# Kernel optimization log

Measured on AMD Instinct MI355X. Metric: run time of the kernel, lower is better.

The kernel has to match this reference:

```python
import jax, jax.numpy as jnp
import numpy as np

NUM_HEADS = 32
KV_HEADS = 8
HEAD_SIZE = 128
BATCH = 32
BLOCK_SIZE = 16
BLOCKS_PER_SEQ = 128
NUM_BLOCKS = BATCH * BLOCKS_PER_SEQ  # 4096
ROPE_BASE = 10000.0


def _rope(x, pos):
    # x: [B, n_heads, D]; pos: [B] int32 -> rotate per-sequence single token
    d = x.shape[-1]
    inv_freq = 1.0 / (ROPE_BASE ** (jnp.arange(0, d, 2, dtype=jnp.float32) / d))  # [D/2]
    freqs = pos.astype(jnp.float32)[:, None] * inv_freq[None, :]                  # [B, D/2]
    emb = jnp.concatenate([freqs, freqs], axis=-1)                                # [B, D]
    cos = jnp.cos(emb)[:, None, :]
    sin = jnp.sin(emb)[:, None, :]
    x1, x2 = x[..., : d // 2], x[..., d // 2 :]
    rotated = jnp.concatenate([-x2, x1], axis=-1)
    return x * cos + rotated * sin


def setup_inputs() -> dict:
    key = jax.random.key(0)
    ks = jax.random.split(key, 6)
    query = jax.random.normal(ks[0], (BATCH, NUM_HEADS, HEAD_SIZE), dtype=jnp.float32)
    k_new = jax.random.normal(ks[1], (BATCH, KV_HEADS, HEAD_SIZE), dtype=jnp.float32)
    v_new = jax.random.normal(ks[2], (BATCH, KV_HEADS, HEAD_SIZE), dtype=jnp.float32)
    k_cache = jax.random.normal(ks[3], (NUM_BLOCKS, BLOCK_SIZE, KV_HEADS, HEAD_SIZE), dtype=jnp.float32)
    v_cache = jax.random.normal(ks[4], (NUM_BLOCKS, BLOCK_SIZE, KV_HEADS, HEAD_SIZE), dtype=jnp.float32)
    # each sequence owns a contiguous run of blocks
    block_tables = jnp.arange(NUM_BLOCKS, dtype=jnp.int32).reshape(BATCH, BLOCKS_PER_SEQ)
    context_lens = jax.random.randint(ks[5], (BATCH,), 0, 2047, dtype=jnp.int32)
    return {
        "query": query,
        "key": k_new,
        "value": v_new,
        "k_cache": k_cache,
        "v_cache": v_cache,
        "block_tables": block_tables,
        "context_lens": context_lens,
    }


def reference(query, key, value, k_cache, v_cache, block_tables, context_lens):
    B, H, D = query.shape
    KVH = key.shape[1]
    G = H // KVH
    scale = 1.0 / (D ** 0.5)

    # --- RoPE: source uses position = context_len + 1 for both q and k ---
    pos = context_lens + 1
    q = _rope(query, pos)   # [B, H, D]
    k = _rope(key, pos)     # [B, KVH, D]

    # --- scatter new token into the paged KV cache at slot = context_len ---
    slot = context_lens                               # [B]
    blk = jnp.take_along_axis(block_tables, (slot // BLOCK_SIZE)[:, None], axis=1)[:, 0]
    off = slot % BLOCK_SIZE
    k_cache = k_cache.at[blk, off].set(k)
    v_cache = v_cache.at[blk, off].set(value)

    # --- gather this batch's pages: [B, T, KVH, D] with T = blocks*block_size ---
    T = BLOCKS_PER_SEQ * BLOCK_SIZE
    K = k_cache[block_tables].reshape(B, T, KVH, D)
    V = v_cache[block_tables].reshape(B, T, KVH, D)

    # --- GQA single-query attention over cache_seqlens = context_len + 1 ---
    qg = q.reshape(B, KVH, G, D)
    scores = jnp.einsum("bhgd,bthd->bhgt", qg, K) * scale            # [B, KVH, G, T]
    valid = (jnp.arange(T, dtype=jnp.int32)[None, :] < (context_lens + 1)[:, None])
    scores = jnp.where(valid[:, None, None, :], scores, -jnp.inf)
    probs = jax.nn.softmax(scores, axis=-1)
    out = jnp.einsum("bhgt,bthd->bhgd", probs, V)                    # [B, KVH, G, D]
    return out.reshape(B, H, D)
```

## Files before the change

kernel.cpp:

```cpp
#include <hip/hip_runtime.h>
#include <math.h>

#define BATCH    32
#define NHEADS   32
#define KVHEADS  8
#define GRP      4
#define HSZ      128
#define BLKSZ    16
#define BPS      128
#define NTHREADS 512
#define NPROC    16
#define CHUNK    256
#define NSPLIT   8
#define SCALE    0.08838834764831843f

__device__ __forceinline__ void dot4(float4& acc, const float* qb, const float4 k) {
    const float4 qa = *(const float4*)(qb);
    const float4 qg = *(const float4*)(qb + HSZ);
    const float4 qc = *(const float4*)(qb + 2 * HSZ);
    const float4 qd = *(const float4*)(qb + 3 * HSZ);
    acc.x = fmaf(qa.x,k.x,fmaf(qa.y,k.y,fmaf(qa.z,k.z,fmaf(qa.w,k.w,acc.x))));
    acc.y = fmaf(qg.x,k.x,fmaf(qg.y,k.y,fmaf(qg.z,k.z,fmaf(qg.w,k.w,acc.y))));
    acc.z = fmaf(qc.x,k.x,fmaf(qc.y,k.y,fmaf(qc.z,k.z,fmaf(qc.w,k.w,acc.z))));
    acc.w = fmaf(qd.x,k.x,fmaf(qd.y,k.y,fmaf(qd.z,k.z,fmaf(qd.w,k.w,acc.w))));
}

__device__ __forceinline__ void red2(float4& a) {
    a.x += __shfl_xor(a.x,1); a.x += __shfl_xor(a.x,2);
    a.y += __shfl_xor(a.y,1); a.y += __shfl_xor(a.y,2);
    a.z += __shfl_xor(a.z,1); a.z += __shfl_xor(a.z,2);
    a.w += __shfl_xor(a.w,1); a.w += __shfl_xor(a.w,2);
}

__device__ __forceinline__ void pvfma(float4* o, const float4 pv, const float4 vv) {
    o[0].x += pv.x*vv.x; o[0].y += pv.x*vv.y; o[0].z += pv.x*vv.z; o[0].w += pv.x*vv.w;
    o[1].x += pv.y*vv.x; o[1].y += pv.y*vv.y; o[1].z += pv.y*vv.z; o[1].w += pv.y*vv.w;
    o[2].x += pv.z*vv.x; o[2].y += pv.z*vv.y; o[2].z += pv.z*vv.z; o[2].w += pv.z*vv.w;
    o[3].x += pv.w*vv.x; o[3].y += pv.w*vv.y; o[3].z += pv.w*vv.z; o[3].w += pv.w*vv.w;
}

__global__ __launch_bounds__(NTHREADS, 8) void pa_partial(
    const float* __restrict__ query,
    const float* __restrict__ k_new,
    const float* __restrict__ v_new,
    const float* __restrict__ k_cache,
    const float* __restrict__ v_cache,
    const int*  __restrict__ block_tables,
    const int*  __restrict__ ctx_lens,
    float* __restrict__ pm, float* __restrict__ pl, float* __restrict__ po)
{
    const int wg    = blockIdx.x;
    const int chunk = wg & (NSPLIT - 1);
    const int kvh   = (wg >> 3) & (KVHEADS - 1);
    const int b     = wg >> 6;
    const int ctx   = ctx_lens[b];
    const int t0    = chunk * CHUNK;
    if (t0 > ctx) return;

    const int tid  = threadIdx.x;
    const int lane = tid & 63;
    const int wave = tid >> 6;

    __shared__ float q_s[GRP][HSZ];
    __shared__ float kn_s[HSZ];
    __shared__ int   bt_s[CHUNK / BLKSZ];
    __shared__ float sp[CHUNK][GRP];
    __shared__ float redm[8], redl[8];
    __shared__ float o_s[NPROC][GRP][HSZ];

    {
        float* s1 = &sp[0][0];
        s1[tid]       = -INFINITY;
        s1[tid + 512] = -INFINITY;
    }
    {
        const float p = (float)(ctx + 1);
        if (tid < 320) {
            const int   i    = tid & 63;
            const float invf = exp2f(-((float)i / 64.0f) * 13.287712379549449f);
            float s_, c_;
            sincosf(p * invf, &s_, &c_);
            if (tid < 256) {
                const int g = tid >> 6;
                const float* qp = query + ((size_t)b * NHEADS + kvh * GRP + g) * HSZ;
                const float x1 = qp[i], x2 = qp[i + 64];
                q_s[g][i]      = (x1 * c_ - x2 * s_) * SCALE;
                q_s[g][i + 64] = (x2 * c_ + x1 * s_) * SCALE;
            } else {
                const float* kp = k_new + ((size_t)b * KVHEADS + kvh) * HSZ;
                const float x1 = kp[i], x2 = kp[i + 64];
                kn_s[i]      = x1 * c_ - x2 * s_;
                kn_s[i + 64] = x2 * c_ + x1 * s_;
            }
        } else if (tid < 320 + CHUNK / BLKSZ) {
            bt_s[tid - 320] = block_tables[b * BPS + (t0 >> 4) + (tid - 320)];
        }
    }
    __syncthreads();

    const int ncache = min(t0 + CHUNK, ctx) - t0;

    const int rg = lane >> 2;
    const int j  = lane & 3;
    const int jo = j << 2;

    {
        const int tA0 = wave * 16;
        const int tB0 = 128 + wave * 16;
        if (tB0 < ncache) {
            const float* kra = k_cache + (((size_t)bt_s[tA0 >> 4] * BLKSZ + rg) * KVHEADS + kvh) * HSZ + jo;
            const float* krb = k_cache + (((size_t)bt_s[tB0 >> 4] * BLKSZ + rg) * KVHEADS + kvh) * HSZ + jo;
            float4 ka[8], kb[8];
#pragma unroll
            for (int u = 0; u < 8; ++u) ka[u] = *(const float4*)(kra + u * 16);
#pragma unroll
            for (int u = 0; u < 8; ++u) kb[u] = *(const float4*)(krb + u * 16);
            float4 aA = make_float4(0.f,0.f,0.f,0.f);
            float4 aB = make_float4(0.f,0.f,0.f,0.f);
#pragma unroll
            for (int u = 0; u < 8; ++u) {
                const float* qb = &q_s[0][u * 16 + jo];
                dot4(aA, qb, ka[u]);
                dot4(aB, qb, kb[u]);
            }
            red2(aA); red2(aB);
            if (j == 0) {
                *(float4*)&sp[tA0 + rg][0] = aA;
                if (tB0 + rg < ncache) *(float4*)&sp[tB0 + rg][0] = aB;
            }
        } else if (tA0 < ncache) {
            const float* kra = k_cache + (((size_t)bt_s[tA0 >> 4] * BLKSZ + rg) * KVHEADS + kvh) * HSZ + jo;
            float4 ka[8];
#pragma unroll
            for (int u = 0; u < 8; ++u) ka[u] = *(const float4*)(kra + u * 16);
            float4 aA = make_float4(0.f,0.f,0.f,0.f);
#pragma unroll
            for (int u = 0; u < 8; ++u) dot4(aA, &q_s[0][u * 16 + jo], ka[u]);
            red2(aA);
            if (j == 0 && tA0 + rg < ncache) *(float4*)&sp[tA0 + rg][0] = aA;
        }
    }
    if (chunk == (ctx >> 8) && wave == 0) {
        const int tc = ctx - t0;
        float4 acc = make_float4(0.f,0.f,0.f,0.f);
#pragma unroll
        for (int u = 0; u < 8; ++u) {
            const float4 kv = *(const float4*)&kn_s[u * 16 + jo];
            dot4(acc, &q_s[0][u * 16 + jo], kv);
        }
        red2(acc);
        if (lane == 0) *(float4*)&sp[tc][0] = acc;
    }
    __syncthreads();

    const int g2 = tid >> 7;
    const int t2 = (tid & 127) << 1;
    const float a0 = sp[t2][g2], a1 = sp[t2 + 1][g2];
    float mx = fmaxf(a0, a1);
    mx = fmaxf(mx, __shfl_xor(mx, 1));
    mx = fmaxf(mx, __shfl_xor(mx, 2));
    mx = fmaxf(mx, __shfl_xor(mx, 4));
    mx = fmaxf(mx, __shfl_xor(mx, 8));
    mx = fmaxf(mx, __shfl_xor(mx, 16));
    mx = fmaxf(mx, __shfl_xor(mx, 32));
    if ((tid & 63) == 0) redm[tid >> 6] = mx;
    __syncthreads();
    const float m_g = fmaxf(redm[g2 << 1], redm[(g2 << 1) + 1]);
    const float p0 = __expf(a0 - m_g);
    const float p1 = __expf(a1 - m_g);
    sp[t2][g2]     = p0;
    sp[t2 + 1][g2] = p1;
    float ls = p0 + p1;
    ls += __shfl_xor(ls, 1);
    ls += __shfl_xor(ls, 2);
    ls += __shfl_xor(ls, 4);
    ls += __shfl_xor(ls, 8);
    ls += __shfl_xor(ls, 16);
    ls += __shfl_xor(ls, 32);
    if ((tid & 63) == 0) redl[tid >> 6] = ls;
    __syncthreads();
    const float l_g = redl[g2 << 1] + redl[(g2 << 1) + 1];

    const int sub  = tid & 31;
    const int proc = tid >> 5;
    const int d0   = sub << 2;
    float4 o[GRP];
#pragma unroll
    for (int g = 0; g < GRP; ++g) o[g] = make_float4(0.f,0.f,0.f,0.f);
    {
        float4 v0 = make_float4(0.f,0.f,0.f,0.f);
        float4 v1 = v0;
        #define VADDR(tt, fb) (v_cache + (((size_t)bt_s[(((tt) < ncache) ? (tt) : (fb)) >> 4] * BLKSZ \
                              + ((((tt) < ncache) ? (tt) : (fb)) & 15)) * KVHEADS + kvh) * HSZ + d0)
        if (proc < ncache) {
            v0 = *(const float4*)VADDR(proc, proc);
            v1 = *(const float4*)VADDR(proc + 16, proc);
            for (int t = proc; t < ncache; t += NPROC) {
                const float4 vn = *(const float4*)VADDR(t + 32, t);
                const float4 pv = *(const float4*)&sp[t][0];
                pvfma(o, pv, v0);
                v0 = v1; v1 = vn;
            }
        }
        #undef VADDR
    }
    if (chunk == (ctx >> 8)) {
        const int tc = ctx - t0;
        if (proc == (tc & (NPROC - 1))) {
            const float4 vn = *(const float4*)(v_new + ((size_t)b * KVHEADS + kvh) * HSZ + d0);
            const float4 pv = *(const float4*)&sp[tc][0];
            pvfma(o, pv, vn);
        }
    }

#pragma unroll
    for (int g = 0; g < GRP; ++g) *(float4*)&o_s[proc][g][d0] = o[g];
    __syncthreads();
    {
        const int g = tid >> 7;
        const int d = tid & 127;
        float acc = 0.f;
#pragma unroll
        for (int p = 0; p < NPROC; ++p) acc += o_s[p][g][d];
        const size_t idx = (((size_t)(b * KVHEADS + kvh)) * GRP + g) * NSPLIT + chunk;
        if (d == 0) { pm[idx] = m_g; pl[idx] = l_g; }
        po[idx * HSZ + d] = acc;
    }
}

__global__ __launch_bounds__(NTHREADS) void pa_reduce(
    const int*  __restrict__ ctx_lens,
    const float* __restrict__ pm, const float* __restrict__ pl,
    const float* __restrict__ po, float* __restrict__ out)
{
    const int b    = blockIdx.x >> 3;
    const int kvh  = blockIdx.x & 7;
    const int ctx  = ctx_lens[b];
    const int nact = (ctx >> 8) + 1;
    const int tid  = threadIdx.x;
    const int g    = tid >> 7;
    const int d    = tid & 127;
    const size_t idx = (((size_t)(b * KVHEADS + kvh)) * GRP + g) * NSPLIT;

    float M = -INFINITY;
    for (int p = 0; p < nact; ++p) M = fmaxf(M, pm[idx + p]);
    float L = 0.f, O = 0.f;
    for (int p = 0; p < nact; ++p) {
        const float w = __expf(pm[idx + p] - M);
        L += pl[idx + p] * w;
        O += po[(idx + p) * HSZ + d] * w;
    }
    out[((size_t)b * NHEADS + kvh * GRP + g) * HSZ + d] = O / L;
}

__device__ __forceinline__ float hsum32(float v) {
    v += __shfl_xor(v, 1); v += __shfl_xor(v, 2); v += __shfl_xor(v, 4);
    v += __shfl_xor(v, 8); v += __shfl_xor(v, 16);
    return v;
}
__device__ __forceinline__ void proc_row_f(const float4 kv, const float4 vv,
                                           const float4* qf, float* m, float* l, float4* o) {
    float s[GRP];
#pragma unroll
    for (int g = 0; g < GRP; ++g)
        s[g] = qf[g].x*kv.x + qf[g].y*kv.y + qf[g].z*kv.z + qf[g].w*kv.w;
#pragma unroll
    for (int g = 0; g < GRP; ++g) s[g] = hsum32(s[g]);
#pragma unroll
    for (int g = 0; g < GRP; ++g) {
        const float sc = s[g] * SCALE;
        const float mn = fmaxf(m[g], sc);
        const float cf = __expf(m[g] - mn);
        const float pp = __expf(sc - mn);
        l[g] = l[g] * cf + pp;
        o[g].x = o[g].x*cf + pp*vv.x; o[g].y = o[g].y*cf + pp*vv.y;
        o[g].z = o[g].z*cf + pp*vv.z; o[g].w = o[g].w*cf + pp*vv.w;
        m[g] = mn;
    }
}
__global__ __launch_bounds__(NTHREADS) void paged_attn_single(
    const float* __restrict__ query, const float* __restrict__ k_new,
    const float* __restrict__ v_new, const float* __restrict__ k_cache,
    const float* __restrict__ v_cache, const int* __restrict__ block_tables,
    const int* __restrict__ ctx_lens, float* __restrict__ out)
{
    const int wg = blockIdx.x, b = wg >> 3, kvh = wg & 7;
    const int tid = threadIdx.x, sub = tid & 31, proc = tid >> 5;
    const int ctx = ctx_lens[b];
    __shared__ float q_s[GRP][HSZ];
    __shared__ float kn_s[HSZ];
    __shared__ int   bt_s[BPS];
    __shared__ float m_s[16][GRP];
    __shared__ float l_s[16][GRP];
    __shared__ float o_s[16][GRP][HSZ];
    {
        const float p = (float)(ctx + 1);
        if (tid < 320) {
            const int   i    = tid & 63;
            const float invf = exp2f(-((float)i / 64.0f) * 13.287712379549449f);
            float s_, c_;
            sincosf(p * invf, &s_, &c_);
            if (tid < 256) {
                const int g = tid >> 6;
                const float* qp = query + ((size_t)b * NHEADS + kvh * GRP + g) * HSZ;
                const float x1 = qp[i], x2 = qp[i + 64];
                q_s[g][i] = x1*c_ - x2*s_; q_s[g][i+64] = x2*c_ + x1*s_;
            } else {
                const float* kp = k_new + ((size_t)b * KVHEADS + kvh) * HSZ;
                const float x1 = kp[i], x2 = kp[i + 64];
                kn_s[i] = x1*c_ - x2*s_; kn_s[i+64] = x2*c_ + x1*s_;
            }
        } else if (tid < 448) {
            bt_s[tid - 320] = block_tables[b * BPS + (tid - 320)];
        }
    }
    __syncthreads();
    const int d0 = sub << 2;
    float4 qf[GRP];
#pragma unroll
    for (int g = 0; g < GRP; ++g) qf[g] = *(const float4*)&q_s[g][d0];
    float m[GRP], l[GRP]; float4 o[GRP];
#pragma unroll
    for (int g = 0; g < GRP; ++g) { m[g] = -INFINITY; l[g] = 0.f; o[g] = make_float4(0,0,0,0); }
    for (int t = proc; t < ctx; t += 16) {
        const int blk = bt_s[t >> 4];
        const size_t a0 = (((size_t)blk*BLKSZ + (t & 15))*KVHEADS + kvh)*HSZ + d0;
        proc_row_f(*(const float4*)(k_cache + a0), *(const float4*)(v_cache + a0), qf, m, l, o);
    }
    if (proc == (ctx & 15)) {
        proc_row_f(*(const float4*)&kn_s[d0],
                   *(const float4*)(v_new + ((size_t)b*KVHEADS + kvh)*HSZ + d0), qf, m, l, o);
    }
    if (sub == 0) {
#pragma unroll
        for (int g = 0; g < GRP; ++g) { m_s[proc][g] = m[g]; l_s[proc][g] = l[g]; }
    }
#pragma unroll
    for (int g = 0; g < GRP; ++g) *(float4*)&o_s[proc][g][d0] = o[g];
    __syncthreads();
    {
        const int g = tid >> 7, d = tid & 127;
        float mt = -INFINITY;
#pragma unroll
        for (int p = 0; p < 16; ++p) mt = fmaxf(mt, m_s[p][g]);
        float lt = 0.f, ot = 0.f;
#pragma unroll
        for (int p = 0; p < 16; ++p) {
            const float wgt = __expf(m_s[p][g] - mt);
            lt += l_s[p][g]*wgt; ot += o_s[p][g][d]*wgt;
        }
        out[((size_t)b*NHEADS + kvh*GRP + g)*HSZ + d] = ot / lt;
    }
}

extern "C" void kernel_launch(void* const* d_in, const int* in_sizes, int n_in,
                              void* d_out, int out_size, void* d_ws, size_t ws_size,
                              hipStream_t stream) {
    const float* query        = (const float*)d_in[0];
    const float* k_new        = (const float*)d_in[1];
    const float* v_new        = (const float*)d_in[2];
    const float* k_cache      = (const float*)d_in[3];
    const float* v_cache      = (const float*)d_in[4];
    const int*   block_tables = (const int*)d_in[5];
    const int*   ctx_lens     = (const int*)d_in[6];
    float*       out          = (float*)d_out;

    const size_t NPART = (size_t)BATCH * KVHEADS * GRP * NSPLIT;
    const size_t need  = (NPART * 2 + NPART * HSZ) * sizeof(float);

    if (ws_size >= need) {
        float* pm = (float*)d_ws;
        float* pl = pm + NPART;
        float* po = pl + NPART;
        pa_partial<<<dim3(BATCH * KVHEADS * NSPLIT), dim3(NTHREADS), 0, stream>>>(
            query, k_new, v_new, k_cache, v_cache, block_tables, ctx_lens, pm, pl, po);
        pa_reduce<<<dim3(BATCH * KVHEADS), dim3(NTHREADS), 0, stream>>>(
            ctx_lens, pm, pl, po, out);
    } else {
        paged_attn_single<<<dim3(BATCH * KVHEADS), dim3(NTHREADS), 0, stream>>>(
            query, k_new, v_new, k_cache, v_cache, block_tables, ctx_lens, out);
    }
}
```

Measured before the change: 72.56 us.

## Split context into 64-token chunks and stage V in shared memory

Splits each sequence into 32 chunks of 64 tokens instead of 8 chunks of 256, and uses 256-thread workgroups, giving many more workgroups for latency hiding across the GPU. Each thread loads its K and V rows together in one pass, and V is staged in shared memory for the PV product. This replaces the separate strided V-prefetch loop and cross-wave o_s reduction. Softmax is now done per wave with a single 64-lane reduction. The cost is four times more partials for the reduce kernel and a larger workspace, which may trigger the single-kernel fallback if the workspace is too small.

```diff
diff --git a/kernel.cpp b/kernel.cpp
--- a/kernel.cpp
+++ b/kernel.cpp
@@ -8,11 +8,12 @@
 #define HSZ      128
 #define BLKSZ    16
 #define BPS      128
-#define NTHREADS 512
-#define NPROC    16
-#define CHUNK    256
-#define NSPLIT   8
+#define NTHREADS 256
+#define CHUNK    64
+#define NSPLIT   32
 #define SCALE    0.08838834764831843f
+
+#define NPART    ((size_t)BATCH * KVHEADS * GRP * NSPLIT)
 
 __device__ __forceinline__ void dot4(float4& acc, const float* qb, const float4 k) {
     const float4 qa = *(const float4*)(qb);
@@ -32,14 +33,7 @@
     a.w += __shfl_xor(a.w,1); a.w += __shfl_xor(a.w,2);
 }
 
-__device__ __forceinline__ void pvfma(float4* o, const float4 pv, const float4 vv) {
-    o[0].x += pv.x*vv.x; o[0].y += pv.x*vv.y; o[0].z += pv.x*vv.z; o[0].w += pv.x*vv.w;
-    o[1].x += pv.y*vv.x; o[1].y += pv.y*vv.y; o[1].z += pv.y*vv.z; o[1].w += pv.y*vv.w;
-    o[2].x += pv.z*vv.x; o[2].y += pv.z*vv.y; o[2].z += pv.z*vv.z; o[2].w += pv.z*vv.w;
-    o[3].x += pv.w*vv.x; o[3].y += pv.w*vv.y; o[3].z += pv.w*vv.z; o[3].w += pv.w*vv.w;
-}
-
-__global__ __launch_bounds__(NTHREADS, 8) void pa_partial(
+__global__ __launch_bounds__(NTHREADS, 4) void pa_partial(
     const float* __restrict__ query,
     const float* __restrict__ k_new,
     const float* __restrict__ v_new,
@@ -49,186 +43,128 @@
     const int*  __restrict__ ctx_lens,
     float* __restrict__ pm, float* __restrict__ pl, float* __restrict__ po)
 {
-    const int wg    = blockIdx.x;
-    const int chunk = wg & (NSPLIT - 1);
-    const int kvh   = (wg >> 3) & (KVHEADS - 1);
-    const int b     = wg >> 6;
+    const int chunk = blockIdx.x & (NSPLIT - 1);
+    const int kvh   = (blockIdx.x >> 5) & (KVHEADS - 1);
+    const int b     = blockIdx.x >> 8;
     const int ctx   = ctx_lens[b];
     const int t0    = chunk * CHUNK;
     if (t0 > ctx) return;
 
     const int tid  = threadIdx.x;
     const int lane = tid & 63;
-    const int wave = tid >> 6;
+    const int w    = tid >> 6;
 
     __shared__ float q_s[GRP][HSZ];
     __shared__ float kn_s[HSZ];
+    __shared__ float vt[CHUNK][HSZ + 4];
+    __shared__ float sp[CHUNK][GRP];
     __shared__ int   bt_s[CHUNK / BLKSZ];
-    __shared__ float sp[CHUNK][GRP];
-    __shared__ float redm[8], redl[8];
-    __shared__ float o_s[NPROC][GRP][HSZ];
-
-    {
-        float* s1 = &sp[0][0];
-        s1[tid]       = -INFINITY;
-        s1[tid + 512] = -INFINITY;
-    }
-    {
-        const float p = (float)(ctx + 1);
-        if (tid < 320) {
-            const int   i    = tid & 63;
-            const float invf = exp2f(-((float)i / 64.0f) * 13.287712379549449f);
-            float s_, c_;
-            sincosf(p * invf, &s_, &c_);
-            if (tid < 256) {
-                const int g = tid >> 6;
-                const float* qp = query + ((size_t)b * NHEADS + kvh * GRP + g) * HSZ;
-                const float x1 = qp[i], x2 = qp[i + 64];
-                q_s[g][i]      = (x1 * c_ - x2 * s_) * SCALE;
-                q_s[g][i + 64] = (x2 * c_ + x1 * s_) * SCALE;
-            } else {
-                const float* kp = k_new + ((size_t)b * KVHEADS + kvh) * HSZ;
-                const float x1 = kp[i], x2 = kp[i + 64];
-                kn_s[i]      = x1 * c_ - x2 * s_;
-                kn_s[i + 64] = x2 * c_ + x1 * s_;
-            }
-        } else if (tid < 320 + CHUNK / BLKSZ) {
-            bt_s[tid - 320] = block_tables[b * BPS + (t0 >> 4) + (tid - 320)];
-        }
-    }
-    __syncthreads();
-
-    const int ncache = min(t0 + CHUNK, ctx) - t0;
+
+    {
+        const int   i    = tid & 63;
+        const float p    = (float)(ctx + 1);
+        const float invf = exp2f(-((float)i / 64.0f) * 13.287712379549449f);
+        float s_, c_;
+        sincosf(p * invf, &s_, &c_);
+        const int g = tid >> 6;
+        const float* qp = query + ((size_t)b * NHEADS + kvh * GRP + g) * HSZ;
+        const float x1 = qp[i], x2 = qp[i + 64];
+        q_s[g][i]      = (x1 * c_ - x2 * s_) * SCALE;
+        q_s[g][i + 64] = (x2 * c_ + x1 * s_) * SCALE;
+        if (tid < 64) {
+            const float* kp = k_new + ((size_t)b * KVHEADS + kvh) * HSZ;
+            const float y1 = kp[i], y2 = kp[i + 64];
+            kn_s[i]      = y1 * c_ - y2 * s_;
+            kn_s[i + 64] = y2 * c_ + y1 * s_;
+        }
+        if (tid < CHUNK / BLKSZ) bt_s[tid] = block_tables[b * BPS + chunk * (CHUNK / BLKSZ) + tid];
+    }
+    __syncthreads();
+
+    const int  nvalid  = min(CHUNK, ctx - t0 + 1);
+    const bool has_new = (chunk == (ctx >> 6));
+    const int  tc      = ctx - t0;
 
     const int rg = lane >> 2;
     const int j  = lane & 3;
     const int jo = j << 2;
-
-    {
-        const int tA0 = wave * 16;
-        const int tB0 = 128 + wave * 16;
-        if (tB0 < ncache) {
-            const float* kra = k_cache + (((size_t)bt_s[tA0 >> 4] * BLKSZ + rg) * KVHEADS + kvh) * HSZ + jo;
-            const float* krb = k_cache + (((size_t)bt_s[tB0 >> 4] * BLKSZ + rg) * KVHEADS + kvh) * HSZ + jo;
-            float4 ka[8], kb[8];
-#pragma unroll
-            for (int u = 0; u < 8; ++u) ka[u] = *(const float4*)(kra + u * 16);
-#pragma unroll
-            for (int u = 0; u < 8; ++u) kb[u] = *(const float4*)(krb + u * 16);
-            float4 aA = make_float4(0.f,0.f,0.f,0.f);
-            float4 aB = make_float4(0.f,0.f,0.f,0.f);
-#pragma unroll
-            for (int u = 0; u < 8; ++u) {
-                const float* qb = &q_s[0][u * 16 + jo];
-                dot4(aA, qb, ka[u]);
-                dot4(aB, qb, kb[u]);
-            }
-            red2(aA); red2(aB);
-            if (j == 0) {
-                *(float4*)&sp[tA0 + rg][0] = aA;
-                if (tB0 + rg < ncache) *(float4*)&sp[tB0 + rg][0] = aB;
-            }
-        } else if (tA0 < ncache) {
-            const float* kra = k_cache + (((size_t)bt_s[tA0 >> 4] * BLKSZ + rg) * KVHEADS + kvh) * HSZ + jo;
-            float4 ka[8];
-#pragma unroll
-            for (int u = 0; u < 8; ++u) ka[u] = *(const float4*)(kra + u * 16);
-            float4 aA = make_float4(0.f,0.f,0.f,0.f);
-#pragma unroll
-            for (int u = 0; u < 8; ++u) dot4(aA, &q_s[0][u * 16 + jo], ka[u]);
-            red2(aA);
-            if (j == 0 && tA0 + rg < ncache) *(float4*)&sp[tA0 + rg][0] = aA;
-        }
-    }
-    if (chunk == (ctx >> 8) && wave == 0) {
-        const int tc = ctx - t0;
-        float4 acc = make_float4(0.f,0.f,0.f,0.f);
-#pragma unroll
-        for (int u = 0; u < 8; ++u) {
-            const float4 kv = *(const float4*)&kn_s[u * 16 + jo];
-            dot4(acc, &q_s[0][u * 16 + jo], kv);
-        }
+    const int t  = w * 16 + rg;
+    const int tcl = min(t, nvalid - 1);
+
+    {
+        const size_t rowbase = (((size_t)bt_s[tcl >> 4] * BLKSZ + (tcl & 15)) * KVHEADS + kvh) * (size_t)HSZ;
+        const float* kr = k_cache + rowbase + jo;
+        const float* vr = (has_new && tcl == tc)
+                        ? (v_new + ((size_t)b * KVHEADS + kvh) * HSZ + jo)
+                        : (v_cache + rowbase + jo);
+        float4 ka[8], va[8];
+#pragma unroll
+        for (int u = 0; u < 8; ++u) ka[u] = *(const float4*)(kr + u * 16);
+#pragma unroll
+        for (int u = 0; u < 8; ++u) va[u] = *(const float4*)(vr + u * 16);
+
+        float4 acc = make_float4(0.f, 0.f, 0.f, 0.f);
+#pragma unroll
+        for (int u = 0; u < 8; ++u) dot4(acc, &q_s[0][u * 16 + jo], ka[u]);
         red2(acc);
-        if (lane == 0) *(float4*)&sp[tc][0] = acc;
-    }
-    __syncthreads();
-
-    const int g2 = tid >> 7;
-    const int t2 = (tid & 127) << 1;
-    const float a0 = sp[t2][g2], a1 = sp[t2 + 1][g2];
-    float mx = fmaxf(a0, a1);
-    mx = fmaxf(mx, __shfl_xor(mx, 1));
-    mx = fmaxf(mx, __shfl_xor(mx, 2));
-    mx = fmaxf(mx, __shfl_xor(mx, 4));
-    mx = fmaxf(mx, __shfl_xor(mx, 8));
-    mx = fmaxf(mx, __shfl_xor(mx, 16));
-    mx = fmaxf(mx, __shfl_xor(mx, 32));
-    if ((tid & 63) == 0) redm[tid >> 6] = mx;
-    __syncthreads();
-    const float m_g = fmaxf(redm[g2 << 1], redm[(g2 << 1) + 1]);
-    const float p0 = __expf(a0 - m_g);
-    const float p1 = __expf(a1 - m_g);
-    sp[t2][g2]     = p0;
-    sp[t2 + 1][g2] = p1;
-    float ls = p0 + p1;
-    ls += __shfl_xor(ls, 1);
-    ls += __shfl_xor(ls, 2);
-    ls += __shfl_xor(ls, 4);
-    ls += __shfl_xor(ls, 8);
-    ls += __shfl_xor(ls, 16);
-    ls += __shfl_xor(ls, 32);
-    if ((tid & 63) == 0) redl[tid >> 6] = ls;
-    __syncthreads();
-    const float l_g = redl[g2 << 1] + redl[(g2 << 1) + 1];
-
-    const int sub  = tid & 31;
-    const int proc = tid >> 5;
-    const int d0   = sub << 2;
-    float4 o[GRP];
-#pragma unroll
-    for (int g = 0; g < GRP; ++g) o[g] = make_float4(0.f,0.f,0.f,0.f);
-    {
-        float4 v0 = make_float4(0.f,0.f,0.f,0.f);
-        float4 v1 = v0;
-        #define VADDR(tt, fb) (v_cache + (((size_t)bt_s[(((tt) < ncache) ? (tt) : (fb)) >> 4] * BLKSZ \
-                              + ((((tt) < ncache) ? (tt) : (fb)) & 15)) * KVHEADS + kvh) * HSZ + d0)
-        if (proc < ncache) {
-            v0 = *(const float4*)VADDR(proc, proc);
-            v1 = *(const float4*)VADDR(proc + 16, proc);
-            for (int t = proc; t < ncache; t += NPROC) {
-                const float4 vn = *(const float4*)VADDR(t + 32, t);
-                const float4 pv = *(const float4*)&sp[t][0];
-                pvfma(o, pv, v0);
-                v0 = v1; v1 = vn;
-            }
-        }
-        #undef VADDR
-    }
-    if (chunk == (ctx >> 8)) {
-        const int tc = ctx - t0;
-        if (proc == (tc & (NPROC - 1))) {
-            const float4 vn = *(const float4*)(v_new + ((size_t)b * KVHEADS + kvh) * HSZ + d0);
-            const float4 pv = *(const float4*)&sp[tc][0];
-            pvfma(o, pv, vn);
-        }
-    }
-
-#pragma unroll
-    for (int g = 0; g < GRP; ++g) *(float4*)&o_s[proc][g][d0] = o[g];
-    __syncthreads();
-    {
-        const int g = tid >> 7;
-        const int d = tid & 127;
-        float acc = 0.f;
-#pragma unroll
-        for (int p = 0; p < NPROC; ++p) acc += o_s[p][g][d];
-        const size_t idx = (((size_t)(b * KVHEADS + kvh)) * GRP + g) * NSPLIT + chunk;
-        if (d == 0) { pm[idx] = m_g; pl[idx] = l_g; }
-        po[idx * HSZ + d] = acc;
-    }
-}
-
-__global__ __launch_bounds__(NTHREADS) void pa_reduce(
+        if (j == 0 && t < nvalid) *(float4*)&sp[t][0] = acc;
+
+#pragma unroll
+        for (int u = 0; u < 8; ++u) *(float4*)&vt[t][u * 16 + jo] = va[u];
+    }
+    if (has_new && w == (tc >> 4) && rg == (tc & 15)) {
+        float4 acc = make_float4(0.f, 0.f, 0.f, 0.f);
+#pragma unroll
+        for (int u = 0; u < 8; ++u) dot4(acc, &q_s[0][u * 16 + jo], *(const float4*)&kn_s[u * 16 + jo]);
+        red2(acc);
+        if (j == 0) *(float4*)&sp[tc][0] = acc;
+    }
+    __syncthreads();
+
+    {
+        const int tt = lane;
+        float sc = sp[tt][w];
+        if (tt >= nvalid) sc = -INFINITY;
+        float mx = sc;
+#pragma unroll
+        for (int hop = 1; hop <= 32; hop <<= 1) mx = fmaxf(mx, __shfl_xor(mx, hop));
+        const float pr = __expf(sc - mx);
+        float ls = pr;
+#pragma unroll
+        for (int hop = 1; hop <= 32; hop <<= 1) ls += __shfl_xor(ls, hop);
+        sp[tt][w] = pr;
+        if (lane == 0) {
+            const size_t idx = (((size_t)(b * KVHEADS + kvh)) * GRP + w) * NSPLIT + chunk;
+            pm[idx] = mx; pl[idx] = ls;
+        }
+    }
+    __syncthreads();
+
+    {
+        const int d0 = lane << 1;
+        float2 oe = make_float2(0.f, 0.f), oo = make_float2(0.f, 0.f);
+#pragma unroll 8
+        for (int tt = 0; tt + 1 < nvalid; tt += 2) {
+            const float p0 = sp[tt][w];
+            const float p1 = sp[tt + 1][w];
+            const float2 v0 = *(const float2*)&vt[tt][d0];
+            const float2 v1 = *(const float2*)&vt[tt + 1][d0];
+            oe.x = fmaf(p0, v0.x, oe.x); oe.y = fmaf(p0, v0.y, oe.y);
+            oo.x = fmaf(p1, v1.x, oo.x); oo.y = fmaf(p1, v1.y, oo.y);
+        }
+        if (nvalid & 1) {
+            const int tt = nvalid - 1;
+            const float p0 = sp[tt][w];
+            const float2 v0 = *(const float2*)&vt[tt][d0];
+            oe.x = fmaf(p0, v0.x, oe.x); oe.y = fmaf(p0, v0.y, oe.y);
+        }
+        const size_t idx = (((size_t)(b * KVHEADS + kvh)) * GRP + w) * NSPLIT + chunk;
+        float2 o = make_float2(oe.x + oo.x, oe.y + oo.y);
+        *(float2*)&po[idx * HSZ + d0] = o;
+    }
+}
+
+__global__ __launch_bounds__(512) void pa_reduce(
     const int*  __restrict__ ctx_lens,
     const float* __restrict__ pm, const float* __restrict__ pl,
     const float* __restrict__ po, float* __restrict__ out)
@@ -236,7 +172,7 @@
     const int b    = blockIdx.x >> 3;
     const int kvh  = blockIdx.x & 7;
     const int ctx  = ctx_lens[b];
-    const int nact = (ctx >> 8) + 1;
+    const int nact = (ctx >> 6) + 1;
     const int tid  = threadIdx.x;
     const int g    = tid >> 7;
     const int d    = tid & 127;
@@ -278,7 +214,7 @@
         m[g] = mn;
     }
 }
-__global__ __launch_bounds__(NTHREADS) void paged_attn_single(
+__global__ __launch_bounds__(512) void paged_attn_single(
     const float* __restrict__ query, const float* __restrict__ k_new,
     const float* __restrict__ v_new, const float* __restrict__ k_cache,
     const float* __restrict__ v_cache, const int* __restrict__ block_tables,
@@ -365,8 +301,7 @@
     const int*   ctx_lens     = (const int*)d_in[6];
     float*       out          = (float*)d_out;
 
-    const size_t NPART = (size_t)BATCH * KVHEADS * GRP * NSPLIT;
-    const size_t need  = (NPART * 2 + NPART * HSZ) * sizeof(float);
+    const size_t need = (NPART * 2 + NPART * HSZ) * sizeof(float);
 
     if (ws_size >= need) {
         float* pm = (float*)d_ws;
@@ -374,10 +309,10 @@
         float* po = pl + NPART;
         pa_partial<<<dim3(BATCH * KVHEADS * NSPLIT), dim3(NTHREADS), 0, stream>>>(
             query, k_new, v_new, k_cache, v_cache, block_tables, ctx_lens, pm, pl, po);
-        pa_reduce<<<dim3(BATCH * KVHEADS), dim3(NTHREADS), 0, stream>>>(
+        pa_reduce<<<dim3(BATCH * KVHEADS), dim3(512), 0, stream>>>(
             ctx_lens, pm, pl, po, out);
     } else {
-        paged_attn_single<<<dim3(BATCH * KVHEADS), dim3(NTHREADS), 0, stream>>>(
+        paged_attn_single<<<dim3(BATCH * KVHEADS), dim3(512), 0, stream>>>(
             query, k_new, v_new, k_cache, v_cache, block_tables, ctx_lens, out);
     }
 }
```

Result: slower. 80.52 us (+11.0%).
